# Kernel tuning notes

Measured on AMD Instinct MI355X. Metric: run time of the kernel, lower is better.

## Reference

```python
import jax, jax.numpy as jnp
import numpy as np

N, D = 8192, 512
NUM_SOURCES = 8


def setup_inputs() -> dict:
    key = jax.random.key(0)
    k1, k2, k3 = jax.random.split(key, 3)
    image_features = jax.random.normal(k1, (N, D), dtype=jnp.float32)
    text_features = jax.random.normal(k2, (N, D), dtype=jnp.float32)
    logit_scale = jnp.ones((), dtype=jnp.float32)
    source_labels = jax.random.randint(k3, (N,), 0, NUM_SOURCES, dtype=jnp.int64)
    return {
        "image_features": image_features,
        "text_features": text_features,
        "logit_scale": logit_scale,
        "source_labels": source_labels,
    }


def reference(image_features, text_features, logit_scale, source_labels):
    n = source_labels.shape[0]
    # [N, N] logits and row-wise log-softmax
    logits = logit_scale * (image_features @ text_features.T)
    log_probs = jax.nn.log_softmax(logits, axis=1)
    # same-source mask, diagonal excluded
    mask = (source_labels[:, None] == source_labels[None, :]) & (~jnp.eye(n, dtype=bool))
    count_pos = mask.sum(axis=1)  # [N]
    row_sum = jnp.where(mask, log_probs, 0.0).sum(axis=1)  # [N]
    # per-row mean over positives; rows with zero positives contribute 0
    row_mean = jnp.where(count_pos > 0, row_sum / jnp.maximum(count_pos, 1).astype(log_probs.dtype), 0.0)
    # loss = -(sum_i row_mean_i) / N
    return -row_mean.sum() / n
```

## Files before the change

### kernel.cpp

```cpp
#include <hip/hip_runtime.h>
#include <cmath>

#define NN 8192
#define DD 512
#define NSRC 8
#define PSW 32
#define COFF 100.0f

typedef __bf16 bf16x8 __attribute__((ext_vector_type(8)));
typedef float  f32x4  __attribute__((ext_vector_type(4)));

__device__ __forceinline__ unsigned short f2bf(float f) {
    unsigned u = __float_as_uint(f);
    u += 0x7fffu + ((u >> 16) & 1u);
    return (unsigned short)(u >> 16);
}

__global__ __launch_bounds__(256) void k_cast(
    const float* __restrict__ img, const float* __restrict__ txt,
    unsigned short* __restrict__ imgB, unsigned short* __restrict__ txtB,
    float* __restrict__ Tsum, int* __restrict__ counts, float* __restrict__ out)
{
    if (blockIdx.x == 0) {
        float4 z = {0.f, 0.f, 0.f, 0.f};
#pragma unroll
        for (int k = 0; k < 4; k++)
            *(float4*)(Tsum + (k * 256 + threadIdx.x) * 4) = z;
        if (threadIdx.x < NSRC) counts[threadIdx.x] = 0;
        if (threadIdx.x == 0) out[0] = 0.f;
    }
    const size_t gid = (size_t)blockIdx.x * 256 + threadIdx.x;
    const size_t half = (size_t)NN * DD / 8;
    const float* src = (gid < half) ? img : txt;
    unsigned short* dst = (gid < half) ? imgB : txtB;
    const size_t off = ((gid < half) ? gid : gid - half) * 8;
    const float4 v0 = *(const float4*)(src + off);
    const float4 v1 = *(const float4*)(src + off + 4);
    union { unsigned short s[8]; uint4 v; } o;
    o.s[0] = f2bf(v0.x); o.s[1] = f2bf(v0.y); o.s[2] = f2bf(v0.z); o.s[3] = f2bf(v0.w);
    o.s[4] = f2bf(v1.x); o.s[5] = f2bf(v1.y); o.s[6] = f2bf(v1.z); o.s[7] = f2bf(v1.w);
    *(uint4*)(dst + off) = o.v;
}

__global__ __launch_bounds__(256) void k_src_sums(
    const float* __restrict__ txt, const int* __restrict__ labels,
    float* __restrict__ Tsum, int* __restrict__ counts)
{
    __shared__ float Tacc[NSRC * DD];
    __shared__ int cacc[NSRC];
    const int tid = threadIdx.x;
    const int d0 = 2 * tid;
#pragma unroll
    for (int s = 0; s < NSRC; s++) {
        Tacc[s * DD + d0] = 0.f;
        Tacc[s * DD + d0 + 1] = 0.f;
    }
    if (tid < NSRC) cacc[tid] = 0;
    __syncthreads();

    const int row0 = blockIdx.x * 64;
    if (tid < 64) atomicAdd(&cacc[labels[row0 + tid]], 1);

    for (int j = 0; j < 64; j++) {
        const int lab = labels[row0 + j];
        const float2 v = *(const float2*)(txt + (size_t)(row0 + j) * DD + d0);
        Tacc[lab * DD + d0]     += v.x;
        Tacc[lab * DD + d0 + 1] += v.y;
    }
    __syncthreads();
#pragma unroll
    for (int k = 0; k < NSRC * DD / 256; k++) {
        const int e = k * 256 + tid;
        atomicAdd(&Tsum[e], Tacc[e]);
    }
    if (tid < NSRC) atomicAdd(&counts[tid], cacc[tid]);
}

__global__ __launch_bounds__(512, 2) void k_lse_mfma256(
    const unsigned short* __restrict__ imgB, const unsigned short* __restrict__ txtB,
    const float* __restrict__ scale_p, float* __restrict__ ps)
{
    __shared__ uint4 lds[8192];
    const float scale = scale_p[0];
    const int tid  = threadIdx.x;
    const int lane = tid & 63;
    const int w    = tid >> 6;
    const int wr   = w >> 2;
    const int wc   = w & 3;
    const int lq   = lane >> 4;
    const int ln   = lane & 15;
    const int by   = blockIdx.x >> 5;
    const int bcol = blockIdx.x & 31;
    const int row0 = by * 256;
    const int col0 = bcol * 256;

    const int st_r  = tid >> 3;
    const int st_kc = (tid & 7) ^ (st_r & 7);
    const int xsw   = ln & 7;

    int rowA[2][4], colB[2][2];
#pragma unroll
    for (int ih = 0; ih < 2; ih++)
#pragma unroll
        for (int ii = 0; ii < 4; ii++)
            rowA[ih][ii] = (wr * 128 + ih * 64 + ii * 16 + ln) * 8;
#pragma unroll
    for (int jh = 0; jh < 2; jh++)
#pragma unroll
        for (int jj = 0; jj < 2; jj++)
            colB[jh][jj] = (wc * 64 + jh * 32 + jj * 16 + ln) * 8;

#define SA(BUF, Q, T)                                                          \
    { const unsigned short* g = imgB + (size_t)(row0 + (Q) * 64 + st_r) * DD   \
          + (((T) & 7) << 6) + (st_kc << 3);                                   \
      __builtin_amdgcn_global_load_lds(                                        \
          (const __attribute__((address_space(1))) void*)g,                    \
          (__attribute__((address_space(3))) void*)                            \
              &lds[(BUF) * 4096 + (Q) * 512 + tid], 16, 0, 0); }
#define SB(BUF, Q, T)                                                          \
    { const unsigned short* g = txtB + (size_t)(col0 + (Q) * 64 + st_r) * DD   \
          + (((T) & 7) << 6) + (st_kc << 3);                                   \
      __builtin_amdgcn_global_load_lds(                                        \
          (const __attribute__((address_space(1))) void*)g,                    \
          (__attribute__((address_space(3))) void*)                            \
              &lds[(BUF) * 4096 + 2048 + (Q) * 512 + tid], 16, 0, 0); }

#define PHASE_(BUF, IH, JH, RA, STG, VM)                                       \
    do {                                                                       \
        if (RA) {                                                              \
            _Pragma("unroll") for (int ii = 0; ii < 4; ii++) {                 \
                _Pragma("unroll") for (int ks = 0; ks < 2; ks++) {             \
                    af[ii][ks] = *reinterpret_cast<const bf16x8*>(             \
                        &lds[(BUF) * 4096 + rowA[IH][ii]                       \
                             + (((ks << 2) + lq) ^ xsw)]);                     \
                }                                                              \
            }                                                                  \
        }                                                                      \
        bf16x8 bf[2][2];                                                       \
        _Pragma("unroll") for (int jj = 0; jj < 2; jj++) {                     \
            _Pragma("unroll") for (int ks = 0; ks < 2; ks++) {                 \
                bf[jj][ks] = *reinterpret_cast<const bf16x8*>(                 \
                    &lds[(BUF) * 4096 + 2048 + colB[JH][jj]                    \
                         + (((ks << 2) + lq) ^ xsw)]);                         \
            }                                                                  \
        }                                                                      \
        STG;                                                                   \
        __builtin_amdgcn_s_barrier();                                          \
        asm volatile("s_waitcnt lgkmcnt(0)" ::: "memory");                     \
        __builtin_amdgcn_sched_barrier(0);                                     \
        __builtin_amdgcn_s_setprio(1);                                         \
        _Pragma("unroll") for (int ks = 0; ks < 2; ks++) {                     \
            _Pragma("unroll") for (int ii = 0; ii < 4; ii++) {                 \
                _Pragma("unroll") for (int jj = 0; jj < 2; jj++) {             \
                    acc[(IH) * 4 + ii][(JH) * 2 + jj] =                        \
                        __builtin_amdgcn_mfma_f32_16x16x32_bf16(               \
                            af[ii][ks], bf[jj][ks],                            \
                            acc[(IH) * 4 + ii][(JH) * 2 + jj], 0, 0, 0);       \
                }                                                              \
            }                                                                  \
        }                                                                      \
        __builtin_amdgcn_s_setprio(0);                                         \
        if (VM) { asm volatile("s_waitcnt vmcnt(2)" ::: "memory"); }           \
        __builtin_amdgcn_s_barrier();                                          \
    } while (0)

#pragma unroll
    for (int q = 0; q < 4; q++) SA(0, q, 0);
#pragma unroll
    for (int q = 0; q < 4; q++) SB(0, q, 0);
    SA(1, 0, 1); SA(1, 2, 1);
    asm volatile("s_waitcnt vmcnt(2)" ::: "memory");
    __builtin_amdgcn_s_barrier();

    f32x4 acc[8][4];
#pragma unroll
    for (int i = 0; i < 8; i++)
#pragma unroll
        for (int j = 0; j < 4; j++) acc[i][j] = (f32x4){0.f, 0.f, 0.f, 0.f};
    bf16x8 af[4][2];

    for (int t0 = 0; t0 < DD / 64; t0 += 2) {
        PHASE_(0, 0, 0, 1, SA(1, 1, t0 + 1); SA(1, 3, t0 + 1), 0);
        PHASE_(0, 0, 1, 0, SB(1, 0, t0 + 1); SB(1, 1, t0 + 1), 0);
        PHASE_(0, 1, 0, 1, SB(1, 2, t0 + 1); SB(1, 3, t0 + 1), 0);
        PHASE_(0, 1, 1, 0, SA(0, 0, t0 + 2); SA(0, 2, t0 + 2), 1);
        PHASE_(1, 0, 0, 1, SA(0, 1, t0 + 2); SA(0, 3, t0 + 2), 0);
        PHASE_(1, 0, 1, 0, SB(0, 0, t0 + 2); SB(0, 1, t0 + 2), 0);
        PHASE_(1, 1, 0, 1, SB(0, 2, t0 + 2); SB(0, 3, t0 + 2), 0);
        PHASE_(1, 1, 1, 0, SA(1, 0, t0 + 3); SA(1, 2, t0 + 3), 1);
    }

    asm volatile("s_waitcnt vmcnt(0)" ::: "memory");
    __syncthreads();

    float* fred = (float*)lds;
#pragma unroll
    for (int i = 0; i < 8; i++) {
#pragma unroll
        for (int rg = 0; rg < 4; rg++) {
            float es = 0.f;
#pragma unroll
            for (int j = 0; j < 4; j++)
                es += __expf(fmaf(acc[i][j][rg], scale, -COFF));
#pragma unroll
            for (int off = 8; off; off >>= 1) es += __shfl_xor(es, off);
            if (ln == 0)
                fred[(wr * 128 + i * 16 + lq * 4 + rg) * 4 + wc] = es;
        }
    }
    __syncthreads();
    if (tid < 256) {
        const float tot = fred[tid * 4] + fred[tid * 4 + 1]
                        + fred[tid * 4 + 2] + fred[tid * 4 + 3];
        ps[(size_t)(row0 + tid) * PSW + bcol] = tot;
    }
#undef SA
#undef SB
#undef PHASE_
}

__global__ __launch_bounds__(256) void k_finalize(
    const float* __restrict__ img, const float* __restrict__ txt,
    const int* __restrict__ labels, const float* __restrict__ scale_p,
    const float* __restrict__ Tsum, const int* __restrict__ counts,
    const float* __restrict__ ps,
    float* __restrict__ out)
{
    const float scale = scale_p[0];
    const int tid = threadIdx.x;
    const int lane = tid & 63;
    const int wave = tid >> 6;
    const int rowBase = blockIdx.x * 16 + wave * 4;
    float local = 0.f;
#pragma unroll
    for (int it = 0; it < 4; it++) {
        const int i = rowBase + it;
        const int lab = labels[i];
        float ds = 0.f, dt = 0.f;
        const float* ip = img + (size_t)i * DD;
        const float* tp = txt + (size_t)i * DD;
        const float* sp = Tsum + lab * DD;
#pragma unroll
        for (int k = lane; k < DD; k += 64) {
            const float a = ip[k];
            ds = fmaf(a, tp[k], ds);
            dt = fmaf(a, sp[k], dt);
        }
        float es = (lane < PSW) ? ps[(size_t)i * PSW + lane] : 0.f;
#pragma unroll
        for (int off = 32; off; off >>= 1) {
            ds += __shfl_xor(ds, off);
            dt += __shfl_xor(dt, off);
            es += __shfl_xor(es, off);
        }
        if (lane == 0) {
            const float lse = COFF + __logf(es);
            const int cnt = counts[lab] - 1;
            if (cnt > 0) {
                const float row_sum = scale * (dt - ds) - (float)cnt * lse;
                local += row_sum / (float)cnt;
            }
        }
    }
    __shared__ float red[4];
    if (lane == 0) red[wave] = local;
    __syncthreads();
    if (tid == 0) {
        const float t = red[0] + red[1] + red[2] + red[3];
        atomicAdd(out, -t / (float)NN);
    }
}

extern "C" void kernel_launch(void* const* d_in, const int* in_sizes, int n_in,
                              void* d_out, int out_size, void* d_ws, size_t ws_size,
                              hipStream_t stream)
{
    const float* img     = (const float*)d_in[0];
    const float* txt     = (const float*)d_in[1];
    const float* scale_p = (const float*)d_in[2];
    const int*   labels  = (const int*)d_in[3];
    float* out = (float*)d_out;

    char* ws = (char*)d_ws;
    float* ps    = (float*)(ws);
    float* Tsum  = (float*)(ws + (1 << 20));
    int*   counts = (int*)(ws + (1 << 20) + NSRC * DD * 4);
    unsigned short* imgB = (unsigned short*)(ws + 2 * 1024 * 1024);
    unsigned short* txtB = (unsigned short*)(ws + 10 * 1024 * 1024);

    k_cast<<<(2 * NN * DD / 8) / 256, 256, 0, stream>>>(img, txt, imgB, txtB,
                                                        Tsum, counts, out);
    k_src_sums<<<NN / 64, 256, 0, stream>>>(txt, labels, Tsum, counts);
    k_lse_mfma256<<<(NN / 256) * (NN / 256), 512, 0, stream>>>(imgB, txtB,
                                                               scale_p, ps);
    k_finalize<<<NN / 16, 256, 0, stream>>>(img, txt, labels, scale_p,
                                            Tsum, counts, ps, out);
}
```

Measured before the change: 180.2 us.

## Make GEMM blocks persistent over 1024 columns and merge cast with source sums

```diff
diff --git a/kernel.cpp b/kernel.cpp
--- a/kernel.cpp
+++ b/kernel.cpp
@@ -4,7 +4,7 @@
 #define NN 8192
 #define DD 512
 #define NSRC 8
-#define PSW 32
+#define PSW 8
 #define COFF 100.0f
 
 typedef __bf16 bf16x8 __attribute__((ext_vector_type(8)));
@@ -16,39 +16,29 @@
     return (unsigned short)(u >> 16);
 }
 
-__global__ __launch_bounds__(256) void k_cast(
+__global__ __launch_bounds__(256) void k_prep(
     const float* __restrict__ img, const float* __restrict__ txt,
+    const int* __restrict__ labels,
     unsigned short* __restrict__ imgB, unsigned short* __restrict__ txtB,
-    float* __restrict__ Tsum, int* __restrict__ counts, float* __restrict__ out)
-{
-    if (blockIdx.x == 0) {
-        float4 z = {0.f, 0.f, 0.f, 0.f};
-#pragma unroll
-        for (int k = 0; k < 4; k++)
-            *(float4*)(Tsum + (k * 256 + threadIdx.x) * 4) = z;
-        if (threadIdx.x < NSRC) counts[threadIdx.x] = 0;
-        if (threadIdx.x == 0) out[0] = 0.f;
-    }
-    const size_t gid = (size_t)blockIdx.x * 256 + threadIdx.x;
-    const size_t half = (size_t)NN * DD / 8;
-    const float* src = (gid < half) ? img : txt;
-    unsigned short* dst = (gid < half) ? imgB : txtB;
-    const size_t off = ((gid < half) ? gid : gid - half) * 8;
-    const float4 v0 = *(const float4*)(src + off);
-    const float4 v1 = *(const float4*)(src + off + 4);
-    union { unsigned short s[8]; uint4 v; } o;
-    o.s[0] = f2bf(v0.x); o.s[1] = f2bf(v0.y); o.s[2] = f2bf(v0.z); o.s[3] = f2bf(v0.w);
-    o.s[4] = f2bf(v1.x); o.s[5] = f2bf(v1.y); o.s[6] = f2bf(v1.z); o.s[7] = f2bf(v1.w);
-    *(uint4*)(dst + off) = o.v;
-}
-
-__global__ __launch_bounds__(256) void k_src_sums(
-    const float* __restrict__ txt, const int* __restrict__ labels,
     float* __restrict__ Tsum, int* __restrict__ counts)
 {
+    const int tid = threadIdx.x;
+    if (blockIdx.x >= 128) {
+        const size_t gid = (size_t)(blockIdx.x - 128) * 256 + tid;
+        const size_t half = (size_t)NN * DD / 8;
+        const float* src = (gid < half) ? img : txt;
+        unsigned short* dst = (gid < half) ? imgB : txtB;
+        const size_t off = ((gid < half) ? gid : gid - half) * 8;
+        const float4 v0 = *(const float4*)(src + off);
+        const float4 v1 = *(const float4*)(src + off + 4);
+        union { unsigned short s[8]; uint4 v; } o;
+        o.s[0] = f2bf(v0.x); o.s[1] = f2bf(v0.y); o.s[2] = f2bf(v0.z); o.s[3] = f2bf(v0.w);
+        o.s[4] = f2bf(v1.x); o.s[5] = f2bf(v1.y); o.s[6] = f2bf(v1.z); o.s[7] = f2bf(v1.w);
+        *(uint4*)(dst + off) = o.v;
+        return;
+    }
     __shared__ float Tacc[NSRC * DD];
     __shared__ int cacc[NSRC];
-    const int tid = threadIdx.x;
     const int d0 = 2 * tid;
 #pragma unroll
     for (int s = 0; s < NSRC; s++) {
@@ -89,10 +79,12 @@
     const int wc   = w & 3;
     const int lq   = lane >> 4;
     const int ln   = lane & 15;
-    const int by   = blockIdx.x >> 5;
-    const int bcol = blockIdx.x & 31;
-    const int row0 = by * 256;
-    const int col0 = bcol * 256;
+    const int c    = blockIdx.x & 7;
+    const int l    = blockIdx.x >> 3;
+    const int by   = c * 4 + (l >> 3);
+    const int bcg  = l & 7;
+    const int row0    = by * 256;
+    const int colBase = bcg * 1024;
 
     const int st_r  = tid >> 3;
     const int st_kc = (tid & 7) ^ (st_r & 7);
@@ -118,7 +110,8 @@
           (__attribute__((address_space(3))) void*)                            \
               &lds[(BUF) * 4096 + (Q) * 512 + tid], 16, 0, 0); }
 #define SB(BUF, Q, T)                                                          \
-    { const unsigned short* g = txtB + (size_t)(col0 + (Q) * 64 + st_r) * DD   \
+    { const unsigned short* g = txtB                                           \
+          + (size_t)(colBase + ((((T) >> 3) & 3) << 8) + (Q) * 64 + st_r) * DD \
           + (((T) & 7) << 6) + (st_kc << 3);                                   \
       __builtin_amdgcn_global_load_lds(                                        \
           (const __attribute__((address_space(1))) void*)g,                    \
@@ -173,21 +166,41 @@
     __builtin_amdgcn_s_barrier();
 
     f32x4 acc[8][4];
-#pragma unroll
-    for (int i = 0; i < 8; i++)
+    f32x4 s_run[8];
+#pragma unroll
+    for (int i = 0; i < 8; i++) {
+        s_run[i] = (f32x4){0.f, 0.f, 0.f, 0.f};
 #pragma unroll
         for (int j = 0; j < 4; j++) acc[i][j] = (f32x4){0.f, 0.f, 0.f, 0.f};
+    }
     bf16x8 af[4][2];
 
-    for (int t0 = 0; t0 < DD / 64; t0 += 2) {
-        PHASE_(0, 0, 0, 1, SA(1, 1, t0 + 1); SA(1, 3, t0 + 1), 0);
-        PHASE_(0, 0, 1, 0, SB(1, 0, t0 + 1); SB(1, 1, t0 + 1), 0);
-        PHASE_(0, 1, 0, 1, SB(1, 2, t0 + 1); SB(1, 3, t0 + 1), 0);
-        PHASE_(0, 1, 1, 0, SA(0, 0, t0 + 2); SA(0, 2, t0 + 2), 1);
-        PHASE_(1, 0, 0, 1, SA(0, 1, t0 + 2); SA(0, 3, t0 + 2), 0);
-        PHASE_(1, 0, 1, 0, SB(0, 0, t0 + 2); SB(0, 1, t0 + 2), 0);
-        PHASE_(1, 1, 0, 1, SB(0, 2, t0 + 2); SB(0, 3, t0 + 2), 0);
-        PHASE_(1, 1, 1, 0, SA(1, 0, t0 + 3); SA(1, 2, t0 + 3), 1);
+#pragma unroll 1
+    for (int v0 = 0; v0 < 32; v0 += 2) {
+        PHASE_(0, 0, 0, 1, SA(1, 1, v0 + 1); SA(1, 3, v0 + 1), 0);
+        PHASE_(0, 0, 1, 0, SB(1, 0, v0 + 1); SB(1, 1, v0 + 1), 0);
+        PHASE_(0, 1, 0, 1, SB(1, 2, v0 + 1); SB(1, 3, v0 + 1), 0);
+        PHASE_(0, 1, 1, 0, SA(0, 0, v0 + 2); SA(0, 2, v0 + 2), 1);
+        PHASE_(1, 0, 0, 1, SA(0, 1, v0 + 2); SA(0, 3, v0 + 2), 0);
+        PHASE_(1, 0, 1, 0, SB(0, 0, v0 + 2); SB(0, 1, v0 + 2), 0);
+        PHASE_(1, 1, 0, 1, SB(0, 2, v0 + 2); SB(0, 3, v0 + 2), 0);
+        PHASE_(1, 1, 1, 0, SA(1, 0, v0 + 3); SA(1, 2, v0 + 3), 1);
+        if ((v0 & 6) == 6) {
+#pragma unroll
+            for (int i = 0; i < 8; i++) {
+#pragma unroll
+                for (int rg = 0; rg < 4; rg++) {
+                    float es = s_run[i][rg];
+#pragma unroll
+                    for (int j = 0; j < 4; j++)
+                        es += __expf(fmaf(acc[i][j][rg], scale, -COFF));
+                    s_run[i][rg] = es;
+                }
+#pragma unroll
+                for (int j = 0; j < 4; j++)
+                    acc[i][j] = (f32x4){0.f, 0.f, 0.f, 0.f};
+            }
+        }
     }
 
     asm volatile("s_waitcnt vmcnt(0)" ::: "memory");
@@ -198,10 +211,7 @@
     for (int i = 0; i < 8; i++) {
 #pragma unroll
         for (int rg = 0; rg < 4; rg++) {
-            float es = 0.f;
-#pragma unroll
-            for (int j = 0; j < 4; j++)
-                es += __expf(fmaf(acc[i][j][rg], scale, -COFF));
+            float es = s_run[i][rg];
 #pragma unroll
             for (int off = 8; off; off >>= 1) es += __shfl_xor(es, off);
             if (ln == 0)
@@ -212,7 +222,7 @@
     if (tid < 256) {
         const float tot = fred[tid * 4] + fred[tid * 4 + 1]
                         + fred[tid * 4 + 2] + fred[tid * 4 + 3];
-        ps[(size_t)(row0 + tid) * PSW + bcol] = tot;
+        ps[(size_t)(row0 + tid) * PSW + bcg] = tot;
     }
 #undef SA
 #undef SB
@@ -283,16 +293,17 @@
 
     char* ws = (char*)d_ws;
     float* ps    = (float*)(ws);
-    float* Tsum  = (float*)(ws + (1 << 20));
-    int*   counts = (int*)(ws + (1 << 20) + NSRC * DD * 4);
+    float* Tsum  = (float*)(ws + (1 << 18));
+    int*   counts = (int*)(ws + (1 << 18) + NSRC * DD * 4);
     unsigned short* imgB = (unsigned short*)(ws + 2 * 1024 * 1024);
     unsigned short* txtB = (unsigned short*)(ws + 10 * 1024 * 1024);
 
-    k_cast<<<(2 * NN * DD / 8) / 256, 256, 0, stream>>>(img, txt, imgB, txtB,
-                                                        Tsum, counts, out);
-    k_src_sums<<<NN / 64, 256, 0, stream>>>(txt, labels, Tsum, counts);
-    k_lse_mfma256<<<(NN / 256) * (NN / 256), 512, 0, stream>>>(imgB, txtB,
-                                                               scale_p, ps);
+    hipMemsetAsync(ws + (1 << 18), 0, NSRC * DD * 4 + 64, stream);
+    hipMemsetAsync(d_out, 0, 4, stream);
+
+    k_prep<<<128 + (2 * NN * DD / 8) / 256, 256, 0, stream>>>(
+        img, txt, labels, imgB, txtB, Tsum, counts);
+    k_lse_mfma256<<<256, 512, 0, stream>>>(imgB, txtB, scale_p, ps);
     k_finalize<<<NN / 16, 256, 0, stream>>>(img, txt, labels, scale_p,
                                             Tsum, counts, ps, out);
 }
```

Result: no change. 177.6 us (-1.4%).
